# Kernel tuning notes

Measured on AMD Instinct MI355X. Metric: run time of the kernel, lower is better.

Reference implementation:

```python
import jax, jax.numpy as jnp
import numpy as np

# Hyperparameters matching init_kwargs
LR = 0.02
AT = 0.3
DSBETA = 0.1
EPS_DS = 0.5

B, D, N = 8192, 1024, 4096


def setup_inputs() -> dict:
    key = jax.random.key(0)
    k0, k1, k2, k3 = jax.random.split(key, 4)
    x = jax.random.normal(k0, (B, D), dtype=jnp.float32)
    weights = jax.random.normal(k1, (N, D), dtype=jnp.float32)
    relevance = jax.random.uniform(k2, (N, D), dtype=jnp.float32)
    moving_avg = jax.random.uniform(k3, (N, D), dtype=jnp.float32)
    node_control = jnp.ones((N,), dtype=jnp.float32)
    return {"x": x, "weights": weights, "relevance": relevance,
            "moving_avg": moving_avg, "node_control": node_control}


def reference(x, weights, relevance, moving_avg, node_control):
    n, d = weights.shape
    # pairwise squared distances [B, N] via one GEMM
    x2 = jnp.sum(x * x, axis=1, keepdims=True)            # [B,1]
    w2 = jnp.sum(weights * weights, axis=1)[None, :]      # [1,N]
    dists = x2 + w2 - 2.0 * jnp.matmul(x, weights.T)      # [B,N]
    # weighted_distance + activation
    rsum = jnp.sum(relevance, axis=1)                     # [N]
    dw = dists * (rsum / d)[None, :]
    dw = jnp.where(jnp.isnan(dw), 0.0, dw)
    act = (rsum[None, :] / (rsum[None, :] + dw + 1e-7)) * node_control[None, :]
    act_max = jnp.max(act, axis=1)                        # [B]
    idx = jnp.argmax(act, axis=1)                         # [B] winner per sample
    # high-activation mask; group samples by winner node (unique_node_diff_vectorized
    # == per-node mean of assigned high samples, done with segment_sum at fixed N)
    high = (act_max >= AT).astype(x.dtype)                # [B]
    counts = jax.ops.segment_sum(high, idx, num_segments=n)               # [N]
    sums = jax.ops.segment_sum(x * high[:, None], idx, num_segments=n)    # [N,D]
    has = (counts > 0).astype(x.dtype)[:, None]           # [N,1] nodes with >=1 high sample
    mean_s = sums / jnp.maximum(counts, 1.0)[:, None]     # [N,D] updatable_samples (dense)
    # update_node math (EMA moving_avg -> relevance -> weight update)
    a = LR * DSBETA
    distance = jnp.abs(mean_s - weights)
    mavg_new = a * distance + (1.0 - a) * moving_avg
    mx = jnp.max(mavg_new, axis=1, keepdims=True)
    mn = jnp.min(mavg_new, axis=1, keepdims=True)
    avg = jnp.mean(mavg_new, axis=1, keepdims=True)
    rel_new = 1.0 / (1.0 + jnp.exp((mavg_new - avg) / (EPS_DS * (mx - mn))))
    rel_new = jnp.where(jnp.isnan(rel_new), 1.0, rel_new)
    w_new = weights + LR * (mean_s - weights)
    # Original returns rows only for unique winning nodes (dynamic shape); here we
    # return fixed-shape [N,D] arrays masked to zero for nodes with no high sample.
    return (mean_s * has, w_new * has, rel_new * has)
```

## Files before the change

kernel.cpp:

```cpp
#include <hip/hip_runtime.h>
#include <stdint.h>


#define B_DIM 8192
#define D_DIM 1024
#define N_DIM 4096
#define ND ((size_t)N_DIM * D_DIM)
#define LRc 0.02f
#define ATc 0.3f
#define EMAc (0.02f * 0.1f)
#define QS 32.0f
#define INV_QS2 (1.0f / (QS * QS))
#define MARGIN_G 10.0f

typedef int intv4 __attribute__((ext_vector_type(4)));

__device__ __forceinline__ void async16(void* lds, const void* g) {
    __builtin_amdgcn_global_load_lds((const __attribute__((address_space(1))) void*)g,
                                     (__attribute__((address_space(3))) void*)lds, 16, 0, 0);
}

__device__ __forceinline__ int q8(float v) {
    return (int)rintf(fminf(fmaxf(v * QS, -127.0f), 127.0f));
}

__device__ __forceinline__ unsigned pack4(float4 v) {
    return (unsigned)(q8(v.x) & 255) | ((unsigned)(q8(v.y) & 255) << 8)
         | ((unsigned)(q8(v.z) & 255) << 16) | ((unsigned)(q8(v.w) & 255) << 24);
}

__global__ __launch_bounds__(256) void prep_k(const float* __restrict__ x, const float* __restrict__ w,
                                              const float* __restrict__ rel,
                                              signed char* __restrict__ xq, signed char* __restrict__ wq,
                                              float* __restrict__ x2p, float* __restrict__ w2p,
                                              float* __restrict__ rsump, float* __restrict__ gbp) {
    const int lane = threadIdx.x & 63, wave = threadIdx.x >> 6;
    const int row = (blockIdx.x << 2) + wave;
    if (row < B_DIM) {
        const float4* xr = (const float4*)(x + (size_t)row * D_DIM);
        unsigned* xqr = (unsigned*)(xq + (size_t)row * D_DIM);
        float ss = 0.f;
#pragma unroll
        for (int j = 0; j < 4; ++j) {
            const float4 v = xr[lane + j * 64];
            ss += v.x * v.x + v.y * v.y + v.z * v.z + v.w * v.w;
            xqr[lane + j * 64] = pack4(v);
        }
#pragma unroll
        for (int o = 32; o; o >>= 1) ss += __shfl_xor(ss, o);
        if (lane == 0) x2p[row] = ss;
    } else {
        const int n = row - B_DIM;
        const float4* wr = (const float4*)(w + (size_t)n * D_DIM);
        const float4* rr = (const float4*)(rel + (size_t)n * D_DIM);
        unsigned* wqr = (unsigned*)(wq + (size_t)n * D_DIM);
        float ss = 0.f, rs = 0.f;
#pragma unroll
        for (int j = 0; j < 4; ++j) {
            const float4 v = wr[lane + j * 64];
            const float4 rv = rr[lane + j * 64];
            ss += v.x * v.x + v.y * v.y + v.z * v.z + v.w * v.w;
            rs += rv.x + rv.y + rv.z + rv.w;
            wqr[lane + j * 64] = pack4(v);
        }
#pragma unroll
        for (int o = 32; o; o >>= 1) { ss += __shfl_xor(ss, o); rs += __shfl_xor(rs, o); }
        if (lane == 0) {
            w2p[n] = ss;
            rsump[n] = rs;
            gbp[n] = ss + (1e-7f * (float)D_DIM) / rs;
        }
    }
}

__global__ __launch_bounds__(256, 2) void gemm_k(const signed char* __restrict__ xq,
                                                 const signed char* __restrict__ wq,
                                                 const float* __restrict__ gbp,
                                                 unsigned short* __restrict__ resq,
                                                 float* __restrict__ tminp) {
    __shared__ int4 As[1024];
    __shared__ int4 Bs[2048];
    const int t = threadIdx.x;
    const int mt = blockIdx.x & 63;
    const int nt = blockIdx.x >> 6;
    const int m0 = mt * 128, n0 = nt * 256;
    const int lane = t & 63, wave = t >> 6;
    const int q = lane >> 4, ln = lane & 15;
    const int wm = wave >> 1, wn = wave & 1;

    intv4 acc[4][8];
#pragma unroll
    for (int i = 0; i < 4; ++i)
#pragma unroll
        for (int j = 0; j < 8; ++j) acc[i][j] = (intv4){0, 0, 0, 0};

    int rrA[4], jjA[4], rrB[8], jjB[8];
#pragma unroll
    for (int s = 0; s < 4; ++s) {
        int L = t + s * 256;
        rrA[s] = L >> 3; jjA[s] = (L & 7) ^ (rrA[s] & 7);
    }
#pragma unroll
    for (int s = 0; s < 8; ++s) {
        int L = t + s * 256;
        rrB[s] = L >> 3; jjB[s] = (L & 7) ^ (rrB[s] & 7);
    }

    const signed char* Ap = xq + (size_t)m0 * D_DIM;
    const signed char* Bp = wq + (size_t)n0 * D_DIM;
    for (int kt = 0; kt < 8; ++kt) {
        const int k0 = kt * 128;
#pragma unroll
        for (int s = 0; s < 4; ++s)
            async16((char*)As + (t + s * 256) * 16, Ap + (size_t)rrA[s] * D_DIM + k0 + jjA[s] * 16);
#pragma unroll
        for (int s = 0; s < 8; ++s)
            async16((char*)Bs + (t + s * 256) * 16, Bp + (size_t)rrB[s] * D_DIM + k0 + jjB[s] * 16);
        __syncthreads();
#pragma unroll
        for (int ks = 0; ks < 2; ++ks) {
            intv4 a[4], b[8];
#pragma unroll
            for (int i = 0; i < 4; ++i) {
                int r = wm * 64 + i * 16 + ln;
                int jx = (ks * 4 + q) ^ (r & 7);
                a[i] = *(const intv4*)((const char*)As + (r * 8 + jx) * 16);
            }
#pragma unroll
            for (int j = 0; j < 8; ++j) {
                int r = wn * 128 + j * 16 + ln;
                int jx = (ks * 4 + q) ^ (r & 7);
                b[j] = *(const intv4*)((const char*)Bs + (r * 8 + jx) * 16);
            }
#pragma unroll
            for (int i = 0; i < 4; ++i)
#pragma unroll
                for (int j = 0; j < 8; ++j)
                    acc[i][j] = __builtin_amdgcn_mfma_i32_16x16x64_i8(a[i], b[j], acc[i][j], 0, 0, 0);
        }
        __syncthreads();
    }

    float gbv[8];
#pragma unroll
    for (int j = 0; j < 8; ++j) gbv[j] = gbp[n0 + wn * 128 + j * 16 + ln];
    const float cf = 2.0f * INV_QS2;
    const int tileA = nt * 4 + wn * 2;
#pragma unroll
    for (int i = 0; i < 4; ++i) {
#pragma unroll
        for (int r = 0; r < 4; ++r) {
            const int m = m0 + wm * 64 + i * 16 + q * 4 + r;
            float g[8];
            float mnA = 3.4e38f, mnB = 3.4e38f;
#pragma unroll
            for (int j = 0; j < 8; ++j) {
                g[j] = gbv[j] - cf * (float)acc[i][j][r];
                if (j < 4) mnA = fminf(mnA, g[j]); else mnB = fminf(mnB, g[j]);
            }
#pragma unroll
            for (int o = 1; o < 16; o <<= 1) {
                mnA = fminf(mnA, __shfl_xor(mnA, o));
                mnB = fminf(mnB, __shfl_xor(mnB, o));
            }
            if (ln == 0) {
                tminp[(size_t)m * 64 + tileA + 0] = mnA;
                tminp[(size_t)m * 64 + tileA + 1] = mnB;
            }
            unsigned uA = 0, uB = 0;
#pragma unroll
            for (int j = 0; j < 4; ++j) {
                int a4 = (int)rintf(g[j] - mnA);
                a4 = (a4 > 15) ? 15 : a4;
                uA |= (unsigned)a4 << (4 * j);
                int b4 = (int)rintf(g[j + 4] - mnB);
                b4 = (b4 > 15) ? 15 : b4;
                uB |= (unsigned)b4 << (4 * j);
            }
            unsigned short* rq = resq + (size_t)m * 1024;
            rq[(tileA + 0) * 16 + ln] = (unsigned short)uA;
            rq[(tileA + 1) * 16 + ln] = (unsigned short)uB;
        }
    }
}

__global__ __launch_bounds__(256) void resolve_k(const unsigned short* __restrict__ resq,
                                                 const float* __restrict__ tminp,
                                                 const float* __restrict__ x2p,
                                                 const float* __restrict__ x, const float* __restrict__ w,
                                                 const float* __restrict__ w2p, const float* __restrict__ rsump,
                                                 const float* __restrict__ ncp,
                                                 int* __restrict__ win) {
    const int lane = threadIdx.x & 63, wave = threadIdx.x >> 6;
    const int b = (blockIdx.x << 2) + wave;
    const float tv = tminp[(size_t)b * 64 + lane];
    float rowmin = tv;
#pragma unroll
    for (int o = 32; o; o >>= 1) rowmin = fminf(rowmin, __shfl_xor(rowmin, o));
    const float th = rowmin + MARGIN_G;
    const float thq = th + 0.5f;
    const unsigned long long tmask = __ballot(tv <= th);
    const float x2v = x2p[b];
    const unsigned short* rrow = resq + (size_t)b * 1024;
    const int nibsh = (lane >> 4) * 4;

    int cnt = 0, myn = -1;
    float myg = 0.0f;
    unsigned long long tm = tmask;
    while (tm) {
        const int tt = __ffsll((long long)tm) - 1;
        tm &= tm - 1;
        const float tb = __shfl(tv, tt);
        const unsigned short pv = rrow[tt * 16 + (lane & 15)];
        const float g = tb + (float)((pv >> nibsh) & 15);
        const bool c = (g <= thq);
        cnt += __popcll(__ballot(c));
        if (c && myn < 0) { myn = tt * 64 + lane; myg = g; }
    }

    if (cnt == 1) {
        if (myn >= 0) {
            const float act = ncp[myn] * (float)D_DIM / ((float)D_DIM + x2v + myg);
            win[b] = (act >= ATc) ? myn : -1;
        }
    } else {
        const float4* xr = (const float4*)(x + (size_t)b * D_DIM);
        float4 xv[4];
#pragma unroll
        for (int j = 0; j < 4; ++j) xv[j] = xr[lane + j * 64];
        float best_act = -1.0f;
        int best_n = N_DIM;
        tm = tmask;
        while (tm) {
            const int tt = __ffsll((long long)tm) - 1;
            tm &= tm - 1;
            const float tb = __shfl(tv, tt);
            const unsigned short pv = rrow[tt * 16 + (lane & 15)];
            const float g = tb + (float)((pv >> nibsh) & 15);
            unsigned long long cm = __ballot(g <= thq);
            while (cm) {
                const int l = __ffsll((long long)cm) - 1;
                cm &= cm - 1;
                const int n = tt * 64 + l;
                const float4* wr = (const float4*)(w + (size_t)n * D_DIM);
                float p = 0.f;
#pragma unroll
                for (int j = 0; j < 4; ++j) {
                    const float4 wv = wr[lane + j * 64];
                    p += xv[j].x * wv.x + xv[j].y * wv.y + xv[j].z * wv.z + xv[j].w * wv.w;
                }
#pragma unroll
                for (int o = 32; o; o >>= 1) p += __shfl_xor(p, o);
                const float dist = x2v + w2p[n] - 2.0f * p;
                const float rs = rsump[n];
                const float dw = dist * rs * (1.0f / (float)D_DIM);
                const float a = rs * ncp[n] / (rs + dw + 1e-7f);
                if (a > best_act || (a == best_act && n < best_n)) { best_act = a; best_n = n; }
            }
        }
        if (lane == 0) win[b] = (best_act >= ATc) ? best_n : -1;
    }
}

__global__ __launch_bounds__(256) void finalize_k(const float* __restrict__ x, const float* __restrict__ w,
                                                  const float* __restrict__ mavg, const int* __restrict__ win,
                                                  float* __restrict__ out) {
    const int n = blockIdx.x, t = threadIdx.x;
    __shared__ unsigned short list[B_DIM];
    __shared__ int cnt;
    __shared__ float smax[4], smin[4], ssum[4];
    if (t == 0) cnt = 0;
    __syncthreads();
    const int4* wp = (const int4*)win;
#pragma unroll
    for (int k = 0; k < 8; ++k) {
        const int4 v = wp[k * 256 + t];
        const int b0 = (k * 256 + t) * 4;
        if (v.x == n) list[atomicAdd(&cnt, 1)] = (unsigned short)(b0 + 0);
        if (v.y == n) list[atomicAdd(&cnt, 1)] = (unsigned short)(b0 + 1);
        if (v.z == n) list[atomicAdd(&cnt, 1)] = (unsigned short)(b0 + 2);
        if (v.w == n) list[atomicAdd(&cnt, 1)] = (unsigned short)(b0 + 3);
    }
    __syncthreads();
    const int c = cnt;
    float4 s = {0.f, 0.f, 0.f, 0.f};
    for (int e = 0; e < c; ++e) {
        const float4 xv = ((const float4*)(x + (size_t)list[e] * D_DIM))[t];
        s.x += xv.x; s.y += xv.y; s.z += xv.z; s.w += xv.w;
    }
    const float has = (c > 0) ? 1.0f : 0.0f;
    const float invc = 1.0f / fmaxf((float)c, 1.0f);
    const size_t base4 = (size_t)n * (D_DIM / 4);
    const float4 wv = ((const float4*)w)[base4 + t];
    const float4 mk = ((const float4*)mavg)[base4 + t];
    float4 ms, mv;
    ms.x = s.x * invc; ms.y = s.y * invc; ms.z = s.z * invc; ms.w = s.w * invc;
    mv.x = EMAc * fabsf(ms.x - wv.x) + (1.0f - EMAc) * mk.x;
    mv.y = EMAc * fabsf(ms.y - wv.y) + (1.0f - EMAc) * mk.y;
    mv.z = EMAc * fabsf(ms.z - wv.z) + (1.0f - EMAc) * mk.z;
    mv.w = EMAc * fabsf(ms.w - wv.w) + (1.0f - EMAc) * mk.w;
    float lmax = fmaxf(fmaxf(mv.x, mv.y), fmaxf(mv.z, mv.w));
    float lmin = fminf(fminf(mv.x, mv.y), fminf(mv.z, mv.w));
    float lsum = mv.x + mv.y + mv.z + mv.w;
#pragma unroll
    for (int o = 32; o; o >>= 1) {
        lmax = fmaxf(lmax, __shfl_xor(lmax, o));
        lmin = fminf(lmin, __shfl_xor(lmin, o));
        lsum += __shfl_xor(lsum, o);
    }
    const int wave = t >> 6, lane = t & 63;
    if (lane == 0) { smax[wave] = lmax; smin[wave] = lmin; ssum[wave] = lsum; }
    __syncthreads();
    const float mx = fmaxf(fmaxf(smax[0], smax[1]), fmaxf(smax[2], smax[3]));
    const float mn = fminf(fminf(smin[0], smin[1]), fminf(smin[2], smin[3]));
    const float avg = (ssum[0] + ssum[1] + ssum[2] + ssum[3]) * (1.0f / (float)D_DIM);
    const float scale = 0.5f * (mx - mn);
    const float invs = (scale > 0.0f) ? 1.0f / scale : 0.0f;
    float4 relv;
    if (scale > 0.0f) {
        relv.x = 1.0f / (1.0f + __expf((mv.x - avg) * invs));
        relv.y = 1.0f / (1.0f + __expf((mv.y - avg) * invs));
        relv.z = 1.0f / (1.0f + __expf((mv.z - avg) * invs));
        relv.w = 1.0f / (1.0f + __expf((mv.w - avg) * invs));
    } else {
        relv.x = relv.y = relv.z = relv.w = 1.0f;
    }
    float4* o0 = (float4*)out;
    float4 r0, r1, r2;
    r0.x = ms.x * has; r0.y = ms.y * has; r0.z = ms.z * has; r0.w = ms.w * has;
    r1.x = (wv.x + LRc * (ms.x - wv.x)) * has;
    r1.y = (wv.y + LRc * (ms.y - wv.y)) * has;
    r1.z = (wv.z + LRc * (ms.z - wv.z)) * has;
    r1.w = (wv.w + LRc * (ms.w - wv.w)) * has;
    r2.x = relv.x * has; r2.y = relv.y * has; r2.z = relv.z * has; r2.w = relv.w * has;
    o0[base4 + t] = r0;
    o0[ND / 4 + base4 + t] = r1;
    o0[2 * (ND / 4) + base4 + t] = r2;
}

extern "C" void kernel_launch(void* const* d_in, const int* in_sizes, int n_in,
                              void* d_out, int out_size, void* d_ws, size_t ws_size,
                              hipStream_t stream) {
    const float* x    = (const float*)d_in[0];
    const float* w    = (const float*)d_in[1];
    const float* rel  = (const float*)d_in[2];
    const float* mavg = (const float*)d_in[3];
    const float* nc   = (const float*)d_in[4];
    float* out = (float*)d_out;

    char* p = (char*)d_ws;
    size_t off = 0;
    auto take = [&](size_t bytes) -> char* {
        char* r = p + off;
        off += (bytes + 255) & ~(size_t)255;
        return r;
    };
    signed char* xq = (signed char*)take((size_t)B_DIM * D_DIM);
    signed char* wq = (signed char*)take((size_t)N_DIM * D_DIM);
    float* x2       = (float*)take((size_t)B_DIM * 4);
    float* w2       = (float*)take((size_t)N_DIM * 4);
    float* rsum     = (float*)take((size_t)N_DIM * 4);
    float* gb       = (float*)take((size_t)N_DIM * 4);
    unsigned short* resq = (unsigned short*)take((size_t)B_DIM * 1024 * 2);
    float* tminp    = (float*)take((size_t)B_DIM * 64 * 4);
    int* win        = (int*)take((size_t)B_DIM * 4);

    prep_k<<<(B_DIM + N_DIM) / 4, 256, 0, stream>>>(x, w, rel, xq, wq, x2, w2, rsum, gb);
    gemm_k<<<1024, 256, 0, stream>>>(xq, wq, gb, resq, tminp);
    resolve_k<<<B_DIM / 4, 256, 0, stream>>>(resq, tminp, x2, x, w, w2, rsum, nc, win);
    finalize_k<<<N_DIM, 256, 0, stream>>>(x, w, mavg, win, out);
}
```

Baseline: 203.9 us.

## Enlarge int8 GEMM tile to 256x256 with double-buffered async LDS loads

Restructures the int8 distance GEMM to use 512-thread blocks computing 256x256 tiles. The global-to-LDS async loads are double-buffered in 128KB of dynamic shared memory, so the next K slice is fetched while MFMAs run on the current one. MFMA sections are wrapped in s_setprio, and the epilogue is adjusted to the new 64-column per-wave layout. The aim is more reuse per loaded byte and hiding of load latency. In exchange, occupancy drops to one block per CU because of the LDS size, and there are only 512 blocks.

```diff
diff --git a/kernel.cpp b/kernel.cpp
--- a/kernel.cpp
+++ b/kernel.cpp
@@ -73,113 +73,115 @@
     }
 }
 
-__global__ __launch_bounds__(256, 2) void gemm_k(const signed char* __restrict__ xq,
+__global__ __launch_bounds__(512, 2) void gemm_k(const signed char* __restrict__ xq,
                                                  const signed char* __restrict__ wq,
                                                  const float* __restrict__ gbp,
                                                  unsigned short* __restrict__ resq,
                                                  float* __restrict__ tminp) {
-    __shared__ int4 As[1024];
-    __shared__ int4 Bs[2048];
+    extern __shared__ char smem[];
     const int t = threadIdx.x;
-    const int mt = blockIdx.x & 63;
-    const int nt = blockIdx.x >> 6;
-    const int m0 = mt * 128, n0 = nt * 256;
+    const int mt = blockIdx.x & 31;
+    const int nt = blockIdx.x >> 5;
+    const int m0 = mt * 256, n0 = nt * 256;
     const int lane = t & 63, wave = t >> 6;
     const int q = lane >> 4, ln = lane & 15;
-    const int wm = wave >> 1, wn = wave & 1;
-
-    intv4 acc[4][8];
-#pragma unroll
-    for (int i = 0; i < 4; ++i)
-#pragma unroll
-        for (int j = 0; j < 8; ++j) acc[i][j] = (intv4){0, 0, 0, 0};
-
-    int rrA[4], jjA[4], rrB[8], jjB[8];
+    const int wm = wave >> 2, wn = wave & 3;
+
+    intv4 acc[8][4];
+#pragma unroll
+    for (int i = 0; i < 8; ++i)
+#pragma unroll
+        for (int j = 0; j < 4; ++j) acc[i][j] = (intv4){0, 0, 0, 0};
+
+    int gOff[4], lOff[4];
 #pragma unroll
     for (int s = 0; s < 4; ++s) {
-        int L = t + s * 256;
-        rrA[s] = L >> 3; jjA[s] = (L & 7) ^ (rrA[s] & 7);
-    }
-#pragma unroll
-    for (int s = 0; s < 8; ++s) {
-        int L = t + s * 256;
-        rrB[s] = L >> 3; jjB[s] = (L & 7) ^ (rrB[s] & 7);
-    }
-
+        const int L = t + s * 512;
+        const int r = L >> 3;
+        gOff[s] = r * D_DIM + ((L & 7) ^ (r & 7)) * 16;
+        lOff[s] = L * 16;
+    }
     const signed char* Ap = xq + (size_t)m0 * D_DIM;
     const signed char* Bp = wq + (size_t)n0 * D_DIM;
+
+    const int baseA = (wm * 128 + ln) * 128;
+    const int baseB = (wn * 64 + ln) * 128;
+
+#define STAGE_KT(kt, slot) do {                                                     \
+        char* sa_ = smem + (slot) * 65536;                                          \
+        const int k0_ = (kt) * 128;                                                 \
+        _Pragma("unroll")                                                           \
+        for (int s_ = 0; s_ < 4; ++s_) async16(sa_ + lOff[s_], Ap + gOff[s_] + k0_);\
+        _Pragma("unroll")                                                           \
+        for (int s_ = 0; s_ < 4; ++s_) async16(sa_ + 32768 + lOff[s_], Bp + gOff[s_] + k0_); \
+    } while (0)
+
+#define COMPUTE_KT(slot) do {                                                       \
+        const char* sa_ = smem + (slot) * 65536;                                    \
+        const char* sb_ = sa_ + 32768;                                              \
+        _Pragma("unroll")                                                           \
+        for (int ks = 0; ks < 2; ++ks) {                                            \
+            const int jx = ((ks * 4 + q) ^ (ln & 7)) * 16;                          \
+            intv4 a[8], b[4];                                                       \
+            _Pragma("unroll")                                                       \
+            for (int i = 0; i < 8; ++i) a[i] = *(const intv4*)(sa_ + baseA + i * 2048 + jx); \
+            _Pragma("unroll")                                                       \
+            for (int j = 0; j < 4; ++j) b[j] = *(const intv4*)(sb_ + baseB + j * 2048 + jx); \
+            __builtin_amdgcn_s_setprio(1);                                          \
+            _Pragma("unroll")                                                       \
+            for (int i = 0; i < 8; ++i)                                             \
+                _Pragma("unroll")                                                   \
+                for (int j = 0; j < 4; ++j)                                         \
+                    acc[i][j] = __builtin_amdgcn_mfma_i32_16x16x64_i8(a[i], b[j], acc[i][j], 0, 0, 0); \
+            __builtin_amdgcn_s_setprio(0);                                          \
+        }                                                                           \
+    } while (0)
+
+    STAGE_KT(0, 0);
+#pragma unroll
     for (int kt = 0; kt < 8; ++kt) {
-        const int k0 = kt * 128;
-#pragma unroll
-        for (int s = 0; s < 4; ++s)
-            async16((char*)As + (t + s * 256) * 16, Ap + (size_t)rrA[s] * D_DIM + k0 + jjA[s] * 16);
-#pragma unroll
-        for (int s = 0; s < 8; ++s)
-            async16((char*)Bs + (t + s * 256) * 16, Bp + (size_t)rrB[s] * D_DIM + k0 + jjB[s] * 16);
-        __syncthreads();
-#pragma unroll
-        for (int ks = 0; ks < 2; ++ks) {
-            intv4 a[4], b[8];
-#pragma unroll
-            for (int i = 0; i < 4; ++i) {
-                int r = wm * 64 + i * 16 + ln;
-                int jx = (ks * 4 + q) ^ (r & 7);
-                a[i] = *(const intv4*)((const char*)As + (r * 8 + jx) * 16);
+        if (kt < 7) {
+            STAGE_KT(kt + 1, (kt + 1) & 1);
+            asm volatile("s_waitcnt vmcnt(8)" ::: "memory");
+        } else {
+            asm volatile("s_waitcnt vmcnt(0)" ::: "memory");
+        }
+        __builtin_amdgcn_s_barrier();
+        COMPUTE_KT(kt & 1);
+        asm volatile("" ::: "memory");
+        __builtin_amdgcn_s_barrier();
+    }
+#undef STAGE_KT
+#undef COMPUTE_KT
+
+    float gbv[4];
+#pragma unroll
+    for (int j = 0; j < 4; ++j) gbv[j] = gbp[n0 + wn * 64 + j * 16 + ln];
+    const float cf = 2.0f * INV_QS2;
+    const int tile64 = nt * 4 + wn;
+#pragma unroll
+    for (int i = 0; i < 8; ++i) {
+#pragma unroll
+        for (int r = 0; r < 4; ++r) {
+            const int m = m0 + wm * 128 + i * 16 + q * 4 + r;
+            float g[4];
+            float mn = 3.4e38f;
+#pragma unroll
+            for (int j = 0; j < 4; ++j) {
+                g[j] = gbv[j] - cf * (float)acc[i][j][r];
+                mn = fminf(mn, g[j]);
             }
 #pragma unroll
-            for (int j = 0; j < 8; ++j) {
-                int r = wn * 128 + j * 16 + ln;
-                int jx = (ks * 4 + q) ^ (r & 7);
-                b[j] = *(const intv4*)((const char*)Bs + (r * 8 + jx) * 16);
+            for (int o = 1; o < 16; o <<= 1) mn = fminf(mn, __shfl_xor(mn, o));
+            if (ln == 0) tminp[(size_t)m * 64 + tile64] = mn;
+            unsigned u = 0;
+#pragma unroll
+            for (int j = 0; j < 4; ++j) {
+                int a4 = (int)rintf(g[j] - mn);
+                a4 = (a4 > 15) ? 15 : a4;
+                u |= (unsigned)a4 << (4 * j);
             }
-#pragma unroll
-            for (int i = 0; i < 4; ++i)
-#pragma unroll
-                for (int j = 0; j < 8; ++j)
-                    acc[i][j] = __builtin_amdgcn_mfma_i32_16x16x64_i8(a[i], b[j], acc[i][j], 0, 0, 0);
-        }
-        __syncthreads();
-    }
-
-    float gbv[8];
-#pragma unroll
-    for (int j = 0; j < 8; ++j) gbv[j] = gbp[n0 + wn * 128 + j * 16 + ln];
-    const float cf = 2.0f * INV_QS2;
-    const int tileA = nt * 4 + wn * 2;
-#pragma unroll
-    for (int i = 0; i < 4; ++i) {
-#pragma unroll
-        for (int r = 0; r < 4; ++r) {
-            const int m = m0 + wm * 64 + i * 16 + q * 4 + r;
-            float g[8];
-            float mnA = 3.4e38f, mnB = 3.4e38f;
-#pragma unroll
-            for (int j = 0; j < 8; ++j) {
-                g[j] = gbv[j] - cf * (float)acc[i][j][r];
-                if (j < 4) mnA = fminf(mnA, g[j]); else mnB = fminf(mnB, g[j]);
-            }
-#pragma unroll
-            for (int o = 1; o < 16; o <<= 1) {
-                mnA = fminf(mnA, __shfl_xor(mnA, o));
-                mnB = fminf(mnB, __shfl_xor(mnB, o));
-            }
-            if (ln == 0) {
-                tminp[(size_t)m * 64 + tileA + 0] = mnA;
-                tminp[(size_t)m * 64 + tileA + 1] = mnB;
-            }
-            unsigned uA = 0, uB = 0;
-#pragma unroll
-            for (int j = 0; j < 4; ++j) {
-                int a4 = (int)rintf(g[j] - mnA);
-                a4 = (a4 > 15) ? 15 : a4;
-                uA |= (unsigned)a4 << (4 * j);
-                int b4 = (int)rintf(g[j + 4] - mnB);
-                b4 = (b4 > 15) ? 15 : b4;
-                uB |= (unsigned)b4 << (4 * j);
-            }
-            unsigned short* rq = resq + (size_t)m * 1024;
-            rq[(tileA + 0) * 16 + ln] = (unsigned short)uA;
-            rq[(tileA + 1) * 16 + ln] = (unsigned short)uB;
+            resq[(size_t)m * 1024 + tile64 * 16 + ln] = (unsigned short)u;
         }
     }
 }
@@ -365,8 +367,15 @@
     float* tminp    = (float*)take((size_t)B_DIM * 64 * 4);
     int* win        = (int*)take((size_t)B_DIM * 4);
 
+    static bool attr_set = false;
+    if (!attr_set) {
+        (void)hipFuncSetAttribute(reinterpret_cast<const void*>(gemm_k),
+                                  hipFuncAttributeMaxDynamicSharedMemorySize, 131072);
+        attr_set = true;
+    }
+
     prep_k<<<(B_DIM + N_DIM) / 4, 256, 0, stream>>>(x, w, rel, xq, wq, x2, w2, rsum, gb);
-    gemm_k<<<1024, 256, 0, stream>>>(xq, wq, gb, resq, tminp);
+    gemm_k<<<512, 512, 131072, stream>>>(xq, wq, gb, resq, tminp);
     resolve_k<<<B_DIM / 4, 256, 0, stream>>>(resq, tminp, x2, x, w, w2, rsum, nc, win);
     finalize_k<<<N_DIM, 256, 0, stream>>>(x, w, mavg, win, out);
 }
```

Result: no change. 207.3 us (+1.7%).
